# Performance work log

Hardware: AMD Instinct MI355X
Metric: run time of the kernel (lower is better)

## Reference

```python
import jax, jax.numpy as jnp
import numpy as np

C_Z = 128
C_H = 128
EPS = 1e-5


def _layer_norm(x, gamma, beta):
    mu = jnp.mean(x, axis=-1, keepdims=True)
    var = jnp.mean(jnp.square(x - mu), axis=-1, keepdims=True)
    return (x - mu) * jax.lax.rsqrt(var + EPS) * gamma + beta


def setup_inputs() -> dict:
    key = jax.random.key(0)
    ks = jax.random.split(key, 8)
    B, N = 1, 512
    s_z = 1.0 / np.sqrt(C_Z)
    s_h = 1.0 / np.sqrt(C_H)
    return {
        "z": jax.random.normal(ks[0], (B, N, N, C_Z), dtype=jnp.float32),
        "mask": jnp.ones((B, N, N), dtype=jnp.float32),
        # linear_ab_p: c_z -> 2*c_hidden
        "w_ab_p": jax.random.normal(ks[1], (2 * C_H, C_Z), dtype=jnp.float32) * s_z,
        "b_ab_p": jnp.zeros((2 * C_H,), dtype=jnp.float32),
        # linear_ab_g: c_z -> 2*c_hidden (gating init)
        "w_ab_g": jax.random.normal(ks[2], (2 * C_H, C_Z), dtype=jnp.float32) * s_z,
        "b_ab_g": jnp.ones((2 * C_H,), dtype=jnp.float32),
        # linear_g: c_z -> c_z (gating init)
        "w_g": jax.random.normal(ks[3], (C_Z, C_Z), dtype=jnp.float32) * s_z,
        "b_g": jnp.ones((C_Z,), dtype=jnp.float32),
        # linear_z: c_hidden -> c_z (final init)
        "w_z": jax.random.normal(ks[4], (C_Z, C_H), dtype=jnp.float32) * s_h,
        "b_z": jnp.zeros((C_Z,), dtype=jnp.float32),
        # layer norms
        "ln_in_g": jnp.ones((C_Z,), dtype=jnp.float32),
        "ln_in_b": jnp.zeros((C_Z,), dtype=jnp.float32),
        "ln_out_g": jnp.ones((C_H,), dtype=jnp.float32),
        "ln_out_b": jnp.zeros((C_H,), dtype=jnp.float32),
    }


def reference(z, mask, w_ab_p, b_ab_p, w_ab_g, b_ab_g, w_g, b_g, w_z, b_z,
              ln_in_g, ln_in_b, ln_out_g, ln_out_b):
    # [B, N, N, C] pair representation; outgoing triangle update
    zn = _layer_norm(z, ln_in_g, ln_in_b)
    m = mask[..., None]  # [B, N, N, 1]
    # gated dual projections: sigmoid(W_g z) * mask * (W_p z)  -> [B, N, N, 2H]
    gate = jax.nn.sigmoid(jnp.einsum("bijc,hc->bijh", zn, w_ab_g) + b_ab_g) * m
    ab = gate * (jnp.einsum("bijc,hc->bijh", zn, w_ab_p) + b_ab_p)
    a, b = jnp.split(ab, 2, axis=-1)  # each [B, N, N, H]
    # outgoing: x[b,i,j,h] = sum_k a[b,i,k,h] * b[b,j,k,h]
    x = jnp.einsum("bikh,bjkh->bijh", a, b)
    x = _layer_norm(x, ln_out_g, ln_out_b)
    out = (jnp.einsum("bijh,ch->bijc", x, w_z) + b_z)
    g = jax.nn.sigmoid(jnp.einsum("bijc,dc->bijd", zn, w_g) + b_g)
    return out * g
```

## Files before the change

kernel.cpp:

```cpp
#include <hip/hip_runtime.h>
#include <math.h>

#define NN 512
#define RR 262144
#define EPS_F 1e-5f

typedef unsigned short u16;
typedef unsigned int u32;
typedef __bf16 bf16x8 __attribute__((ext_vector_type(8)));
typedef float f32x4 __attribute__((ext_vector_type(4)));

__device__ __forceinline__ u16 f2bs(float f) {
  __bf16 h = (__bf16)f;
  return __builtin_bit_cast(u16, h);
}
__device__ __forceinline__ float bs2f(u16 u) {
  return (float)__builtin_bit_cast(__bf16, u);
}
__device__ __forceinline__ float sigmoidf_(float x) {
  return 1.f / (1.f + __expf(-x));
}

__global__ __launch_bounds__(256) void k_wconv(const float* __restrict__ w_ab_p,
                                               const float* __restrict__ w_ab_g,
                                               const float* __restrict__ w_g,
                                               u16* __restrict__ wb) {
  const int u = blockIdx.x * 256 + threadIdx.x;
  const int row = u >> 5;
  const int c4 = (u & 31) * 4;
  const float* src;
  if (row < 512) {
    const int tt = row >> 7, n = row & 127;
    const int srow = tt * 64 + ((n >> 5) << 4) + (n & 15);
    src = (((n >> 4) & 1) ? w_ab_g : w_ab_p) + srow * 128 + c4;
  } else {
    src = w_g + (row - 512) * 128 + c4;
  }
  const float4 v = *(const float4*)src;
  u16 o[4] = {f2bs(v.x), f2bs(v.y), f2bs(v.z), f2bs(v.w)};
  *(uint2*)(wb + row * 128 + c4) = *(uint2*)o;
}

__global__ __launch_bounds__(256) void k_proj(
    const float* __restrict__ z, const float* __restrict__ mask,
    const u16* __restrict__ wb, const float* __restrict__ b_ab_p,
    const float* __restrict__ b_ab_g, const float* __restrict__ b_g,
    const float* __restrict__ ln_g, const float* __restrict__ ln_b,
    u16* __restrict__ a_t, u16* __restrict__ b_t, u16* __restrict__ g_out) {
  __shared__ __align__(16) u16 As[128 * 136];
  __shared__ __align__(16) u16 Bs[128 * 136];
  __shared__ float maskS[128];
  const int t = threadIdx.x;
  const long row0 = (long)blockIdx.x * 128;

  {
    const int row = t >> 1, half = t & 1;
    const float* zr = z + (row0 + row) * 128 + half * 64;
    float vals[64];
    float s = 0.f, sq = 0.f;
#pragma unroll
    for (int i = 0; i < 16; ++i) {
      const float4 v = *(const float4*)(zr + i * 4);
      vals[i * 4 + 0] = v.x;
      vals[i * 4 + 1] = v.y;
      vals[i * 4 + 2] = v.z;
      vals[i * 4 + 3] = v.w;
      s += v.x + v.y + v.z + v.w;
      sq += v.x * v.x + v.y * v.y + v.z * v.z + v.w * v.w;
    }
    s += __shfl_xor(s, 1);
    sq += __shfl_xor(sq, 1);
    const float mu = s * 0.0078125f;
    const float var = sq * 0.0078125f - mu * mu;
    const float rs = rsqrtf(var + EPS_F);
    u16 ob[64];
#pragma unroll
    for (int i = 0; i < 16; ++i) {
      const float4 gg = *(const float4*)(ln_g + half * 64 + i * 4);
      const float4 bb = *(const float4*)(ln_b + half * 64 + i * 4);
      ob[i * 4 + 0] = f2bs((vals[i * 4 + 0] - mu) * rs * gg.x + bb.x);
      ob[i * 4 + 1] = f2bs((vals[i * 4 + 1] - mu) * rs * gg.y + bb.y);
      ob[i * 4 + 2] = f2bs((vals[i * 4 + 2] - mu) * rs * gg.z + bb.z);
      ob[i * 4 + 3] = f2bs((vals[i * 4 + 3] - mu) * rs * gg.w + bb.w);
    }
    uint4* dst = (uint4*)(As + row * 136 + half * 64);
    const uint4* sp = (const uint4*)ob;
#pragma unroll
    for (int i = 0; i < 8; ++i) dst[i] = sp[i];
  }
  if (t < 128) maskS[t] = mask[row0 + t];

  const int lane = t & 63, wv = t >> 6;
  const int quad = lane >> 4, tl = lane & 15;
  const int wm = wv >> 1, wn = wv & 1;

  for (int tt = 0; tt < 5; ++tt) {
    {
      const int n = t >> 1, half = t & 1;
      const uint4* src = (const uint4*)(wb + (tt * 128 + n) * 128 + half * 64);
      uint4* dst = (uint4*)(Bs + n * 136 + half * 64);
#pragma unroll
      for (int i = 0; i < 8; ++i) dst[i] = src[i];
    }
    __syncthreads();

    f32x4 acc[4][4];
#pragma unroll
    for (int mt = 0; mt < 4; ++mt)
#pragma unroll
      for (int nt = 0; nt < 4; ++nt) acc[mt][nt] = (f32x4){0.f, 0.f, 0.f, 0.f};

#pragma unroll
    for (int ks = 0; ks < 4; ++ks) {
      bf16x8 af[4], bfr[4];
#pragma unroll
      for (int mt = 0; mt < 4; ++mt)
        af[mt] = *(const bf16x8*)(As + (wm * 64 + mt * 16 + tl) * 136 + ks * 32 + quad * 8);
#pragma unroll
      for (int nt = 0; nt < 4; ++nt)
        bfr[nt] = *(const bf16x8*)(Bs + (wn * 64 + nt * 16 + tl) * 136 + ks * 32 + quad * 8);
#pragma unroll
      for (int mt = 0; mt < 4; ++mt)
#pragma unroll
        for (int nt = 0; nt < 4; ++nt)
          acc[mt][nt] = __builtin_amdgcn_mfma_f32_16x16x32_bf16(af[mt], bfr[nt], acc[mt][nt], 0, 0, 0);
    }
    __syncthreads();

    if (tt < 4) {
#pragma unroll
      for (int b2 = 0; b2 < 2; ++b2) {
        const int hl = wn * 32 + b2 * 16 + tl;
        const int hg = tt * 64 + hl;
        const float bp = b_ab_p[hg], bg = b_ab_g[hg];
#pragma unroll
        for (int mt = 0; mt < 4; ++mt)
#pragma unroll
          for (int rg = 0; rg < 4; ++rg) {
            const int r = wm * 64 + mt * 16 + quad * 4 + rg;
            const float p = acc[mt][2 * b2][rg] + bp;
            const float gt = acc[mt][2 * b2 + 1][rg] + bg;
            Bs[hl * 136 + r] = f2bs(sigmoidf_(gt) * maskS[r] * p);
          }
      }
      __syncthreads();
      {
        const int hl = t >> 2, qq = t & 3;
        const int hg = tt * 64 + hl;
        u16* dbuf = (tt < 2) ? a_t : b_t;
        const int hb = (tt < 2) ? hg : hg - 128;
        const uint4* src = (const uint4*)(Bs + hl * 136 + qq * 32);
        uint4* dst = (uint4*)(dbuf + (long)hb * RR + row0 + qq * 32);
#pragma unroll
        for (int i = 0; i < 4; ++i) dst[i] = src[i];
      }
      __syncthreads();
    } else {
#pragma unroll
      for (int nt = 0; nt < 4; ++nt) {
        const int c = wn * 64 + nt * 16 + tl;
        const float bgc = b_g[c];
#pragma unroll
        for (int mt = 0; mt < 4; ++mt)
#pragma unroll
          for (int rg = 0; rg < 4; ++rg) {
            const int r = wm * 64 + mt * 16 + quad * 4 + rg;
            g_out[(row0 + r) * (long)128 + c] = f2bs(sigmoidf_(acc[mt][nt][rg] + bgc));
          }
      }
    }
  }
}

__global__ __launch_bounds__(256) void k_tri(const u16* __restrict__ a_t,
                                             const u16* __restrict__ b_t,
                                             u16* __restrict__ x_t) {
  __shared__ __align__(16) u16 As[128 * 72];
  __shared__ __align__(16) u16 Bs[128 * 72];
  const int t = threadIdx.x;
  const int h = blockIdx.y;
  const int i0 = (blockIdx.x >> 2) * 128, j0 = (blockIdx.x & 3) * 128;
  const u16* Ag = a_t + (long)h * RR;
  const u16* Bg = b_t + (long)h * RR;
  const int lane = t & 63, wv = t >> 6;
  const int quad = lane >> 4, tl = lane & 15;
  const int wm = wv >> 1, wn = wv & 1;
  const int chunk = t & 7, rb = t >> 3;

  f32x4 acc[4][4];
#pragma unroll
  for (int mt = 0; mt < 4; ++mt)
#pragma unroll
    for (int nt = 0; nt < 4; ++nt) acc[mt][nt] = (f32x4){0.f, 0.f, 0.f, 0.f};

  for (int kt = 0; kt < 8; ++kt) {
    __syncthreads();
#pragma unroll
    for (int p = 0; p < 4; ++p) {
      const int row = rb + p * 32;
      *(uint4*)(As + row * 72 + chunk * 8) =
          *(const uint4*)(Ag + (long)(i0 + row) * 512 + kt * 64 + chunk * 8);
      *(uint4*)(Bs + row * 72 + chunk * 8) =
          *(const uint4*)(Bg + (long)(j0 + row) * 512 + kt * 64 + chunk * 8);
    }
    __syncthreads();
#pragma unroll
    for (int ks = 0; ks < 2; ++ks) {
      bf16x8 af[4], bfr[4];
#pragma unroll
      for (int mt = 0; mt < 4; ++mt)
        af[mt] = *(const bf16x8*)(As + (wm * 64 + mt * 16 + tl) * 72 + ks * 32 + quad * 8);
#pragma unroll
      for (int nt = 0; nt < 4; ++nt)
        bfr[nt] = *(const bf16x8*)(Bs + (wn * 64 + nt * 16 + tl) * 72 + ks * 32 + quad * 8);
#pragma unroll
      for (int mt = 0; mt < 4; ++mt)
#pragma unroll
        for (int nt = 0; nt < 4; ++nt)
          acc[mt][nt] = __builtin_amdgcn_mfma_f32_16x16x32_bf16(af[mt], bfr[nt], acc[mt][nt], 0, 0, 0);
    }
  }
#pragma unroll
  for (int mt = 0; mt < 4; ++mt)
#pragma unroll
    for (int nt = 0; nt < 4; ++nt)
#pragma unroll
      for (int rg = 0; rg < 4; ++rg) {
        const int i = i0 + wm * 64 + mt * 16 + quad * 4 + rg;
        const int j = j0 + wn * 64 + nt * 16 + tl;
        x_t[(long)h * RR + (long)i * 512 + j] = f2bs(acc[mt][nt][rg]);
      }
}

__global__ __launch_bounds__(256) void k_out(const u16* __restrict__ x_t,
                                             const float* __restrict__ w_z,
                                             const float* __restrict__ b_z,
                                             const float* __restrict__ ln_g,
                                             const float* __restrict__ ln_b,
                                             const u16* __restrict__ g_in,
                                             float* __restrict__ out) {
  __shared__ __align__(16) u16 Xs[128 * 136];
  __shared__ __align__(16) u16 Ws[128 * 136];
  __shared__ float lnGs[128], lnBs[128];
  const int t = threadIdx.x;
  const long row0 = (long)blockIdx.x * 128;

  if (t < 128) {
    lnGs[t] = ln_g[t];
    lnBs[t] = ln_b[t];
  }
  {
    const int hb = t >> 3, rq = t & 7;
    u32 xv[4][8];
#pragma unroll
    for (int hh = 0; hh < 4; ++hh) {
      const uint4* src = (const uint4*)(x_t + (long)(hb * 4 + hh) * RR + row0 + rq * 16);
      const uint4 a = src[0], b = src[1];
      xv[hh][0] = a.x; xv[hh][1] = a.y; xv[hh][2] = a.z; xv[hh][3] = a.w;
      xv[hh][4] = b.x; xv[hh][5] = b.y; xv[hh][6] = b.z; xv[hh][7] = b.w;
    }
#pragma unroll
    for (int rr = 0; rr < 16; ++rr) {
      const int wi = rr >> 1, sh = (rr & 1) * 16;
      const u32 e0 = (xv[0][wi] >> sh) & 0xffffu;
      const u32 e1 = (xv[1][wi] >> sh) & 0xffffu;
      const u32 e2 = (xv[2][wi] >> sh) & 0xffffu;
      const u32 e3 = (xv[3][wi] >> sh) & 0xffffu;
      *(uint2*)(Xs + (rq * 16 + rr) * 136 + hb * 4) = make_uint2(e0 | (e1 << 16), e2 | (e3 << 16));
    }
  }
  {
    const int n = t >> 1, half = t & 1;
    const float* src = w_z + n * 128 + half * 64;
    u16* dst = Ws + n * 136 + half * 64;
#pragma unroll
    for (int i = 0; i < 16; ++i) {
      const float4 v = *(const float4*)(src + i * 4);
      dst[i * 4 + 0] = f2bs(v.x);
      dst[i * 4 + 1] = f2bs(v.y);
      dst[i * 4 + 2] = f2bs(v.z);
      dst[i * 4 + 3] = f2bs(v.w);
    }
  }
  __syncthreads();
  {
    const int r = t >> 1, half = t & 1;
    u16* xr = Xs + r * 136 + half * 64;
    float vals[64];
    float s = 0.f, sq = 0.f;
#pragma unroll
    for (int i = 0; i < 64; ++i) {
      const float v = bs2f(xr[i]);
      vals[i] = v;
      s += v;
      sq += v * v;
    }
    s += __shfl_xor(s, 1);
    sq += __shfl_xor(sq, 1);
    const float mu = s * 0.0078125f;
    const float var = sq * 0.0078125f - mu * mu;
    const float rs = rsqrtf(var + EPS_F);
#pragma unroll
    for (int i = 0; i < 64; ++i) {
      const int hh = half * 64 + i;
      xr[i] = f2bs((vals[i] - mu) * rs * lnGs[hh] + lnBs[hh]);
    }
  }
  __syncthreads();

  const int lane = t & 63, wv = t >> 6;
  const int quad = lane >> 4, tl = lane & 15;
  const int wm = wv >> 1, wn = wv & 1;
  f32x4 acc[4][4];
#pragma unroll
  for (int mt = 0; mt < 4; ++mt)
#pragma unroll
    for (int nt = 0; nt < 4; ++nt) acc[mt][nt] = (f32x4){0.f, 0.f, 0.f, 0.f};

#pragma unroll
  for (int ks = 0; ks < 4; ++ks) {
    bf16x8 af[4], bfr[4];
#pragma unroll
    for (int mt = 0; mt < 4; ++mt)
      af[mt] = *(const bf16x8*)(Xs + (wm * 64 + mt * 16 + tl) * 136 + ks * 32 + quad * 8);
#pragma unroll
    for (int nt = 0; nt < 4; ++nt)
      bfr[nt] = *(const bf16x8*)(Ws + (wn * 64 + nt * 16 + tl) * 136 + ks * 32 + quad * 8);
#pragma unroll
    for (int mt = 0; mt < 4; ++mt)
#pragma unroll
      for (int nt = 0; nt < 4; ++nt)
        acc[mt][nt] = __builtin_amdgcn_mfma_f32_16x16x32_bf16(af[mt], bfr[nt], acc[mt][nt], 0, 0, 0);
  }
#pragma unroll
  for (int nt = 0; nt < 4; ++nt) {
    const int c = wn * 64 + nt * 16 + tl;
    const float bz = b_z[c];
#pragma unroll
    for (int mt = 0; mt < 4; ++mt)
#pragma unroll
      for (int rg = 0; rg < 4; ++rg) {
        const int r = wm * 64 + mt * 16 + quad * 4 + rg;
        const long idx = (row0 + r) * 128 + c;
        out[idx] = (acc[mt][nt][rg] + bz) * bs2f(g_in[idx]);
      }
  }
}

extern "C" void kernel_launch(void* const* d_in, const int* in_sizes, int n_in,
                              void* d_out, int out_size, void* d_ws, size_t ws_size,
                              hipStream_t stream) {
  const float* z = (const float*)d_in[0];
  const float* mask = (const float*)d_in[1];
  const float* w_ab_p = (const float*)d_in[2];
  const float* b_ab_p = (const float*)d_in[3];
  const float* w_ab_g = (const float*)d_in[4];
  const float* b_ab_g = (const float*)d_in[5];
  const float* w_g = (const float*)d_in[6];
  const float* b_g = (const float*)d_in[7];
  const float* w_z = (const float*)d_in[8];
  const float* b_z = (const float*)d_in[9];
  const float* ln_in_g = (const float*)d_in[10];
  const float* ln_in_b = (const float*)d_in[11];
  const float* ln_out_g = (const float*)d_in[12];
  const float* ln_out_b = (const float*)d_in[13];
  float* out = (float*)d_out;

  u16* a_t = (u16*)d_ws;
  u16* b_t = a_t + (size_t)RR * 128;
  u16* x_t = b_t + (size_t)RR * 128;
  u16* g_b = x_t + (size_t)RR * 128;
  u16* wb = g_b + (size_t)RR * 128;

  k_wconv<<<80, 256, 0, stream>>>(w_ab_p, w_ab_g, w_g, wb);
  k_proj<<<RR / 128, 256, 0, stream>>>(z, mask, wb, b_ab_p, b_ab_g, b_g,
                                       ln_in_g, ln_in_b, a_t, b_t, g_b);
  k_tri<<<dim3(16, 128), 256, 0, stream>>>(a_t, b_t, x_t);
  k_out<<<RR / 128, 256, 0, stream>>>(x_t, w_z, b_z, ln_out_g, ln_out_b, g_b, out);
}
```

Baseline: 577.9 us.

## Pre-swizzle projection weights into MFMA fragment order and load directly to registers

Measured after the change: 493.2 us. 1.17x faster.

```diff
diff --git a/kernel.cpp b/kernel.cpp
--- a/kernel.cpp
+++ b/kernel.cpp
@@ -26,29 +26,34 @@
                                                const float* __restrict__ w_g,
                                                u16* __restrict__ wb) {
   const int u = blockIdx.x * 256 + threadIdx.x;
-  const int row = u >> 5;
-  const int c4 = (u & 31) * 4;
+  const int lane = u & 63;
+  const int tl = lane & 15, quad = lane >> 4;
+  const int ks = (u >> 6) & 3, nt = (u >> 8) & 3;
+  const int wn = (u >> 10) & 1, tt = u >> 11;
+  const int n = wn * 64 + nt * 16 + tl;
+  const int k = ks * 32 + quad * 8;
   const float* src;
-  if (row < 512) {
-    const int tt = row >> 7, n = row & 127;
+  if (tt < 4) {
     const int srow = tt * 64 + ((n >> 5) << 4) + (n & 15);
-    src = (((n >> 4) & 1) ? w_ab_g : w_ab_p) + srow * 128 + c4;
+    src = (((n >> 4) & 1) ? w_ab_g : w_ab_p) + srow * 128 + k;
   } else {
-    src = w_g + (row - 512) * 128 + c4;
-  }
-  const float4 v = *(const float4*)src;
-  u16 o[4] = {f2bs(v.x), f2bs(v.y), f2bs(v.z), f2bs(v.w)};
-  *(uint2*)(wb + row * 128 + c4) = *(uint2*)o;
-}
-
-__global__ __launch_bounds__(256) void k_proj(
+    src = w_g + n * 128 + k;
+  }
+  const float4 v0 = *(const float4*)src;
+  const float4 v1 = *(const float4*)(src + 4);
+  u16 o[8] = {f2bs(v0.x), f2bs(v0.y), f2bs(v0.z), f2bs(v0.w),
+              f2bs(v1.x), f2bs(v1.y), f2bs(v1.z), f2bs(v1.w)};
+  *(uint4*)(wb + (long)u * 8) = *(uint4*)o;
+}
+
+__global__ __launch_bounds__(256, 3) void k_proj(
     const float* __restrict__ z, const float* __restrict__ mask,
     const u16* __restrict__ wb, const float* __restrict__ b_ab_p,
     const float* __restrict__ b_ab_g, const float* __restrict__ b_g,
     const float* __restrict__ ln_g, const float* __restrict__ ln_b,
     u16* __restrict__ a_t, u16* __restrict__ b_t, u16* __restrict__ g_out) {
   __shared__ __align__(16) u16 As[128 * 136];
-  __shared__ __align__(16) u16 Bs[128 * 136];
+  __shared__ __align__(16) u16 Ts[64 * 136];
   __shared__ float maskS[128];
   const int t = threadIdx.x;
   const long row0 = (long)blockIdx.x * 128;
@@ -89,20 +94,22 @@
     for (int i = 0; i < 8; ++i) dst[i] = sp[i];
   }
   if (t < 128) maskS[t] = mask[row0 + t];
+  __syncthreads();
 
   const int lane = t & 63, wv = t >> 6;
   const int quad = lane >> 4, tl = lane & 15;
   const int wm = wv >> 1, wn = wv & 1;
 
   for (int tt = 0; tt < 5; ++tt) {
+    bf16x8 bfr[4][4];
     {
-      const int n = t >> 1, half = t & 1;
-      const uint4* src = (const uint4*)(wb + (tt * 128 + n) * 128 + half * 64);
-      uint4* dst = (uint4*)(Bs + n * 136 + half * 64);
-#pragma unroll
-      for (int i = 0; i < 8; ++i) dst[i] = src[i];
-    }
-    __syncthreads();
+      const u16* wsrc = wb + (tt * 2 + wn) * 8192 + lane * 8;
+#pragma unroll
+      for (int nt = 0; nt < 4; ++nt)
+#pragma unroll
+        for (int ks = 0; ks < 4; ++ks)
+          bfr[nt][ks] = *(const bf16x8*)(wsrc + (nt * 4 + ks) * 512);
+    }
 
     f32x4 acc[4][4];
 #pragma unroll
@@ -112,22 +119,19 @@
 
 #pragma unroll
     for (int ks = 0; ks < 4; ++ks) {
-      bf16x8 af[4], bfr[4];
+      bf16x8 af[4];
 #pragma unroll
       for (int mt = 0; mt < 4; ++mt)
         af[mt] = *(const bf16x8*)(As + (wm * 64 + mt * 16 + tl) * 136 + ks * 32 + quad * 8);
 #pragma unroll
-      for (int nt = 0; nt < 4; ++nt)
-        bfr[nt] = *(const bf16x8*)(Bs + (wn * 64 + nt * 16 + tl) * 136 + ks * 32 + quad * 8);
-#pragma unroll
       for (int mt = 0; mt < 4; ++mt)
 #pragma unroll
         for (int nt = 0; nt < 4; ++nt)
-          acc[mt][nt] = __builtin_amdgcn_mfma_f32_16x16x32_bf16(af[mt], bfr[nt], acc[mt][nt], 0, 0, 0);
-    }
-    __syncthreads();
+          acc[mt][nt] = __builtin_amdgcn_mfma_f32_16x16x32_bf16(af[mt], bfr[nt][ks], acc[mt][nt], 0, 0, 0);
+    }
 
     if (tt < 4) {
+      __syncthreads();
 #pragma unroll
       for (int b2 = 0; b2 < 2; ++b2) {
         const int hl = wn * 32 + b2 * 16 + tl;
@@ -140,7 +144,7 @@
             const int r = wm * 64 + mt * 16 + quad * 4 + rg;
             const float p = acc[mt][2 * b2][rg] + bp;
             const float gt = acc[mt][2 * b2 + 1][rg] + bg;
-            Bs[hl * 136 + r] = f2bs(sigmoidf_(gt) * maskS[r] * p);
+            Ts[hl * 136 + r] = f2bs(sigmoidf_(gt) * maskS[r] * p);
           }
       }
       __syncthreads();
@@ -149,12 +153,11 @@
         const int hg = tt * 64 + hl;
         u16* dbuf = (tt < 2) ? a_t : b_t;
         const int hb = (tt < 2) ? hg : hg - 128;
-        const uint4* src = (const uint4*)(Bs + hl * 136 + qq * 32);
+        const uint4* src = (const uint4*)(Ts + hl * 136 + qq * 32);
         uint4* dst = (uint4*)(dbuf + (long)hb * RR + row0 + qq * 32);
 #pragma unroll
         for (int i = 0; i < 4; ++i) dst[i] = src[i];
       }
-      __syncthreads();
     } else {
 #pragma unroll
       for (int nt = 0; nt < 4; ++nt) {
@@ -372,7 +375,7 @@
   u16* g_b = x_t + (size_t)RR * 128;
   u16* wb = g_b + (size_t)RR * 128;
 
-  k_wconv<<<80, 256, 0, stream>>>(w_ab_p, w_ab_g, w_g, wb);
+  k_wconv<<<40, 256, 0, stream>>>(w_ab_p, w_ab_g, w_g, wb);
   k_proj<<<RR / 128, 256, 0, stream>>>(z, mask, wb, b_ab_p, b_ab_g, b_g,
                                        ln_in_g, ln_in_b, a_t, b_t, g_b);
   k_tri<<<dim3(16, 128), 256, 0, stream>>>(a_t, b_t, x_t);
```
